# Optimization experiments

Hardware: AMD Instinct MI355X
Metric: run time of the kernel (lower is better)

Reference implementation:

```python
import jax, jax.numpy as jnp
import numpy as np

N = 100000
E = 1600000
IN_C, HID_C, OUT_C = 64, 128, 64


def sage_conv(x, edge_index, W_l, b_l, W_r):
    # PyG SAGEConv (mean aggr): out = lin_l(mean_{j in N(i)} x_j) + lin_r(x_i)
    src, dst = edge_index[0], edge_index[1]
    n = x.shape[0]
    msg = x[src]                                        # [E, C] gather
    agg = jax.ops.segment_sum(msg, dst, num_segments=n) # [N, C] scatter-add
    deg = jax.ops.segment_sum(jnp.ones((msg.shape[0],), x.dtype), dst, num_segments=n)
    agg = agg / jnp.maximum(deg, 1.0)[:, None]          # mean, deg-0 safe
    return agg @ W_l.T + b_l + x @ W_r.T


def setup_inputs() -> dict:
    key = jax.random.key(0)
    ks = jax.random.split(key, 8)
    x = jax.random.normal(ks[0], (N, IN_C), dtype=jnp.float32)
    edge_index = jax.random.randint(ks[1], (2, E), 0, N)
    s1 = 1.0 / np.sqrt(IN_C)
    s2 = 1.0 / np.sqrt(HID_C)
    W1_l = jax.random.uniform(ks[2], (HID_C, IN_C), jnp.float32, -s1, s1)
    W1_r = jax.random.uniform(ks[3], (HID_C, IN_C), jnp.float32, -s1, s1)
    b1 = jax.random.uniform(ks[4], (HID_C,), jnp.float32, -s1, s1)
    W2_l = jax.random.uniform(ks[5], (OUT_C, HID_C), jnp.float32, -s2, s2)
    W2_r = jax.random.uniform(ks[6], (OUT_C, HID_C), jnp.float32, -s2, s2)
    b2 = jax.random.uniform(ks[7], (OUT_C,), jnp.float32, -s2, s2)
    return {"x": x, "edge_index": edge_index, "W1_l": W1_l, "W1_r": W1_r,
            "b1": b1, "W2_l": W2_l, "W2_r": W2_r, "b2": b2}


def reference(x, edge_index, W1_l, W1_r, b1, W2_l, W2_r, b2):
    h = sage_conv(x, edge_index, W1_l, b1, W1_r)
    h = jax.nn.relu(h)
    h = sage_conv(h, edge_index, W2_l, b2, W2_r)
    return jax.nn.sigmoid(h)
```

## Files before the change

kernel.cpp:

```cpp
#include <hip/hip_runtime.h>
#include <math.h>

#define IN_C 64
#define HID_C 128
#define OUT_C 64
#define NBK 256
#define BD 64
#define GS 16

typedef __attribute__((ext_vector_type(8))) short bf16x8;
typedef __attribute__((ext_vector_type(4))) float f32x4;

__device__ __forceinline__ unsigned short f2bf(float f) {
  unsigned u = __float_as_uint(f);
  u = (u + 0x7FFFu + ((u >> 16) & 1u)) >> 16;
  return (unsigned short)u;
}
__device__ __forceinline__ float bf2f(unsigned v) {
  return __uint_as_float(v << 16);
}
__device__ __forceinline__ unsigned pack2(float a, float b) {
  return (unsigned)f2bf(a) | ((unsigned)f2bf(b) << 16);
}

__global__ __launch_bounds__(256) void k_xb(const int* __restrict__ dst,
                                            int* __restrict__ bh,
                                            const float4* __restrict__ x4,
                                            uint2* __restrict__ xh2,
                                            int E, int Mreal, int Mtot) {
  __shared__ int hh[NBK];
  int t = threadIdx.x;
  if (blockIdx.x < 1024) {
    hh[t] = 0;
    __syncthreads();
    for (int e = blockIdx.x * 256 + t; e < E; e += 1024 * 256)
      atomicAdd(&hh[dst[e] >> 9], 1);
    __syncthreads();
    if (hh[t]) atomicAdd(&bh[t * GS], hh[t]);
  } else {
    int b = blockIdx.x - 1024;
    for (int i = b * 256 + t; i < Mtot; i += 2048 * 256) {
      uint2 p = {0u, 0u};
      if (i < Mreal) {
        float4 v = x4[i];
        p.x = pack2(v.x, v.y);
        p.y = pack2(v.z, v.w);
      }
      xh2[i] = p;
    }
  }
}

__global__ __launch_bounds__(256) void k_bscan(const int* __restrict__ bh,
                                               int* __restrict__ bstart,
                                               int* __restrict__ rstart,
                                               int* __restrict__ gcur) {
  __shared__ int s1[NBK], s2[NBK];
  int t = threadIdx.x;
  int cnt = bh[t * GS];
  int region = 16 * min(cnt, (cnt >> 4) + 512);
  int creg = cnt + 4096;
  s1[t] = region; s2[t] = creg;
  __syncthreads();
  for (int off = 1; off < NBK; off <<= 1) {
    int a1 = (t >= off) ? s1[t - off] : 0;
    int a2 = (t >= off) ? s2[t - off] : 0;
    __syncthreads();
    s1[t] += a1; s2[t] += a2;
    __syncthreads();
  }
  int ex1 = s1[t] - region;
  int ex2 = s2[t] - creg;
  bstart[t] = ex1; gcur[t * GS] = ex1; rstart[t] = ex2;
}

__global__ __launch_bounds__(256) void k_msplit(const int* __restrict__ src,
                                                const int* __restrict__ dst,
                                                int* __restrict__ gcur,
                                                int* __restrict__ ebuf, int E) {
  __shared__ int bcnt[NBK], bhead[NBK];
  __shared__ int bins[BD][NBK];
  int t = threadIdx.x;
  bcnt[t] = 0; bhead[t] = 0;
  int per = (E + gridDim.x - 1) / gridDim.x;
  int e0 = blockIdx.x * per, e1 = min(E, e0 + per);
  int e = e0 + t;
  int pb[8], pv[8]; int pc = 0;
  __syncthreads();
  for (;;) {
    while (pc < 8 && e < e1) {
      int d = dst[e], s = src[e];
      pb[pc] = d >> 9; pv[pc] = (s << 9) | (d & 511);
      pc++; e += 256;
    }
    for (int q = pc - 1; q >= 0; --q) {
      int pos = atomicAdd(&bcnt[pb[q]], 1);
      if (pos < BD) {
        bins[(bhead[pb[q]] + pos) & (BD - 1)][pb[q]] = pv[q];
        pc--;
        if (q != pc) { pb[q] = pb[pc]; pv[q] = pv[pc]; }
      }
    }
    int pending = __syncthreads_count(pc > 0 || e < e1);
    int cntv = min(bcnt[t], BD);
    int head = bhead[t];
    while (cntv >= 16) {
      int base = atomicAdd(&gcur[t * GS], 16);
      int4 o[4];
#pragma unroll
      for (int k = 0; k < 16; ++k)
        ((int*)o)[k] = bins[(head + k) & (BD - 1)][t];
      int4* g = (int4*)(ebuf + base);
      g[0] = o[0]; g[1] = o[1]; g[2] = o[2]; g[3] = o[3];
      head = (head + 16) & (BD - 1);
      cntv -= 16;
    }
    bhead[t] = head;
    bcnt[t] = cntv;
    __syncthreads();
    if (!pending) break;
  }
  int cntv = bcnt[t];
  if (cntv > 0) {
    int head = bhead[t];
    int base = atomicAdd(&gcur[t * GS], 16);
#pragma unroll
    for (int k = 0; k < 16; ++k)
      ebuf[base + k] = (k < cntv) ? bins[(head + k) & (BD - 1)][t] : -1;
  }
}

__global__ __launch_bounds__(512) void k_localcsr(const int* __restrict__ ebuf,
                                                  const int* __restrict__ bstart,
                                                  const int* __restrict__ gcur,
                                                  const int* __restrict__ rstart,
                                                  int* __restrict__ csr,
                                                  int* __restrict__ row_start,
                                                  int* __restrict__ rend,
                                                  float* __restrict__ invd, int N) {
  __shared__ int lcnt[512], loff[512], lcur[512];
  int t = threadIdx.x, b = blockIdx.x;
  int start = bstart[b], endp = gcur[b * GS], rs = rstart[b];
  lcnt[t] = 0;
  __syncthreads();
  for (int i = start + t; i < endp; i += 512) {
    int pe = ebuf[i];
    if (pe != -1) atomicAdd(&lcnt[pe & 511], 1);
  }
  __syncthreads();
  int v = lcnt[t];
  int pvn = (v + 7) & ~7;
  loff[t] = pvn;
  __syncthreads();
  for (int off = 1; off < 512; off <<= 1) {
    int a = (t >= off) ? loff[t - off] : 0;
    __syncthreads();
    loff[t] += a;
    __syncthreads();
  }
  int ex = loff[t] - pvn;
  lcur[t] = ex;
  int node = (b << 9) + t;
  if (node < N) {
    row_start[node] = rs + ex;
    rend[node] = rs + ex + pvn;
    invd[node] = 1.0f / fmaxf((float)v, 1.0f);
  }
  __syncthreads();
  for (int i = start + t; i < endp; i += 512) {
    int pe = ebuf[i];
    if (pe != -1) {
      int pos = atomicAdd(&lcur[pe & 511], 1);
      csr[rs + pos] = pe >> 9;
    }
  }
  for (int k = ex + v; k < ex + pvn; ++k) csr[rs + k] = N;
}

__global__ __launch_bounds__(256) void k_gather1(const uint4* __restrict__ xh4,
                                                 const int* __restrict__ csr,
                                                 const int* __restrict__ row_start,
                                                 const int* __restrict__ rend,
                                                 const float* __restrict__ invd,
                                                 uint4* __restrict__ aggh4, int N) {
  int node = (blockIdx.x * 256 + threadIdx.x) >> 3;
  if (node >= N) return;
  int c = threadIdx.x & 7;
  int lb = threadIdx.x & 56;
  int j = row_start[node], end = rend[node];
  float a0 = 0, a1 = 0, a2 = 0, a3 = 0, a4 = 0, a5 = 0, a6 = 0, a7 = 0;
  for (; j < end; j += 8) {
    int sv = csr[j + c];
#pragma unroll
    for (int k = 0; k < 8; ++k) {
      int s = __shfl(sv, lb + k);
      uint4 v = xh4[s * 8 + c];
      a0 += bf2f(v.x & 0xffffu); a1 += bf2f(v.x >> 16);
      a2 += bf2f(v.y & 0xffffu); a3 += bf2f(v.y >> 16);
      a4 += bf2f(v.z & 0xffffu); a5 += bf2f(v.z >> 16);
      a6 += bf2f(v.w & 0xffffu); a7 += bf2f(v.w >> 16);
    }
  }
  float inv = invd[node];
  uint4 p;
  p.x = pack2(a0 * inv, a1 * inv);
  p.y = pack2(a2 * inv, a3 * inv);
  p.z = pack2(a4 * inv, a5 * inv);
  p.w = pack2(a6 * inv, a7 * inv);
  aggh4[node * 8 + c] = p;
}

__global__ __launch_bounds__(512, 4) void k_lin12(
    const uint4* __restrict__ aggh4, const uint4* __restrict__ xh4,
    const float* __restrict__ W1l, const float* __restrict__ W1r,
    const float* __restrict__ b1, const float* __restrict__ W2l,
    const float* __restrict__ W2r, const float* __restrict__ b2,
    unsigned short* __restrict__ zh, float* __restrict__ r, int N) {
  __shared__ __align__(16) char sA[128 * 256];
  __shared__ __align__(16) char sH[128 * 256];
  int t = threadIdx.x;
  if (blockIdx.x == 0 && t < 32) ((unsigned*)zh)[N * 32 + t] = 0;
  int w = t >> 6, lane = t & 63, qm = lane >> 4, ln = lane & 15;
  bf16x8 w1f[4], w2f[4];
  int o = w * 16 + ln;
#pragma unroll
  for (int kc = 0; kc < 4; ++kc) {
    int k0 = kc * 32 + qm * 8;
    bf16x8 v1, v2;
#pragma unroll
    for (int j = 0; j < 8; ++j) {
      int kk = k0 + j;
      float f1 = (kk < 64) ? W1l[o * 64 + kk] : W1r[o * 64 + (kk - 64)];
      float f2 = (o < 64) ? W2l[o * 128 + kk] : W2r[(o - 64) * 128 + kk];
      v1[j] = (short)f2bf(f1);
      v2[j] = (short)f2bf(f2);
    }
    w1f[kc] = v1; w2f[kc] = v2;
  }
  float4 b1v = *(const float4*)(b1 + w * 16 + qm * 4);
  int u = w * 16 + qm * 4;
  float4 b2v = {0.f, 0.f, 0.f, 0.f};
  if (u >= 64) b2v = *(const float4*)(b2 + (u - 64));

  int ntiles = (N + 127) >> 7;
  for (int tile = blockIdx.x; tile < ntiles; tile += gridDim.x) {
    int base = tile << 7;
#pragma unroll
    for (int rep = 0; rep < 4; ++rep) {
      int i = rep * 512 + t;
      int row = i >> 4, ch = i & 15;
      int node = base + row;
      uint4 v = {0u, 0u, 0u, 0u};
      if (node < N) v = (ch < 8) ? aggh4[node * 8 + ch] : xh4[node * 8 + (ch - 8)];
      *(uint4*)(sA + row * 256 + ((ch * 16) ^ ((row & 7) << 4))) = v;
    }
    __syncthreads();
#pragma unroll
    for (int g = 0; g < 8; ++g) {
      int row = g * 16 + ln;
      int rb = row * 256, sw = (row & 7) << 4;
      f32x4 acc = {0.f, 0.f, 0.f, 0.f};
#pragma unroll
      for (int kc = 0; kc < 4; ++kc) {
        bf16x8 af = *(const bf16x8*)(sA + rb + ((kc * 64 + qm * 16) ^ sw));
        acc = __builtin_amdgcn_mfma_f32_16x16x32_bf16(w1f[kc], af, acc, 0, 0, 0);
      }
      uint2 hp;
      hp.x = pack2(fmaxf(acc[0] + b1v.x, 0.f), fmaxf(acc[1] + b1v.y, 0.f));
      hp.y = pack2(fmaxf(acc[2] + b1v.z, 0.f), fmaxf(acc[3] + b1v.w, 0.f));
      *(uint2*)(sH + rb + ((w * 32 + qm * 8) ^ sw)) = hp;
    }
    __syncthreads();
#pragma unroll
    for (int g = 0; g < 8; ++g) {
      int row = g * 16 + ln;
      int rb = row * 256, sw = (row & 7) << 4;
      f32x4 acc = {0.f, 0.f, 0.f, 0.f};
#pragma unroll
      for (int kc = 0; kc < 4; ++kc) {
        bf16x8 hf = *(const bf16x8*)(sH + rb + ((kc * 64 + qm * 16) ^ sw));
        acc = __builtin_amdgcn_mfma_f32_16x16x32_bf16(w2f[kc], hf, acc, 0, 0, 0);
      }
      int node = base + row;
      if (node < N) {
        if (u < 64) {
          uint2 zv;
          zv.x = pack2(acc[0], acc[1]);
          zv.y = pack2(acc[2], acc[3]);
          *(uint2*)(zh + node * 64 + u) = zv;
        } else {
          float4 rv;
          rv.x = acc[0] + b2v.x; rv.y = acc[1] + b2v.y;
          rv.z = acc[2] + b2v.z; rv.w = acc[3] + b2v.w;
          *(float4*)(r + node * 64 + (u - 64)) = rv;
        }
      }
    }
    __syncthreads();
  }
}

__global__ __launch_bounds__(256) void k_gather2b(const uint4* __restrict__ zh4,
                                                  const float* __restrict__ r,
                                                  const int* __restrict__ csr,
                                                  const int* __restrict__ row_start,
                                                  const int* __restrict__ rend,
                                                  const float* __restrict__ invd,
                                                  float* __restrict__ out, int N) {
  int node = (blockIdx.x * 256 + threadIdx.x) >> 3;
  if (node >= N) return;
  int c = threadIdx.x & 7;
  int lb = threadIdx.x & 56;
  int j = row_start[node], end = rend[node];
  float a0 = 0, a1 = 0, a2 = 0, a3 = 0, a4 = 0, a5 = 0, a6 = 0, a7 = 0;
  for (; j < end; j += 8) {
    int sv = csr[j + c];
#pragma unroll
    for (int k = 0; k < 8; ++k) {
      int s = __shfl(sv, lb + k);
      uint4 v = zh4[s * 8 + c];
      a0 += bf2f(v.x & 0xffffu); a1 += bf2f(v.x >> 16);
      a2 += bf2f(v.y & 0xffffu); a3 += bf2f(v.y >> 16);
      a4 += bf2f(v.z & 0xffffu); a5 += bf2f(v.z >> 16);
      a6 += bf2f(v.w & 0xffffu); a7 += bf2f(v.w >> 16);
    }
  }
  float inv = invd[node];
  const float4* r4 = (const float4*)r;
  float4* o4 = (float4*)out;
  int bi = node * 16 + c * 2;
  float4 r0 = r4[bi], r1 = r4[bi + 1];
  float4 w0, w1;
  w0.x = 1.0f / (1.0f + __expf(-(a0 * inv + r0.x)));
  w0.y = 1.0f / (1.0f + __expf(-(a1 * inv + r0.y)));
  w0.z = 1.0f / (1.0f + __expf(-(a2 * inv + r0.z)));
  w0.w = 1.0f / (1.0f + __expf(-(a3 * inv + r0.w)));
  w1.x = 1.0f / (1.0f + __expf(-(a4 * inv + r1.x)));
  w1.y = 1.0f / (1.0f + __expf(-(a5 * inv + r1.y)));
  w1.z = 1.0f / (1.0f + __expf(-(a6 * inv + r1.z)));
  w1.w = 1.0f / (1.0f + __expf(-(a7 * inv + r1.w)));
  o4[bi] = w0;
  o4[bi + 1] = w1;
}

extern "C" void kernel_launch(void* const* d_in, const int* in_sizes, int n_in,
                              void* d_out, int out_size, void* d_ws, size_t ws_size,
                              hipStream_t stream) {
  const float* x   = (const float*)d_in[0];
  const int*   ei  = (const int*)d_in[1];
  const float* W1l = (const float*)d_in[2];
  const float* W1r = (const float*)d_in[3];
  const float* b1  = (const float*)d_in[4];
  const float* W2l = (const float*)d_in[5];
  const float* W2r = (const float*)d_in[6];
  const float* b2  = (const float*)d_in[7];
  float* out = (float*)d_out;

  int N = in_sizes[0] / IN_C;
  int E = in_sizes[1] / 2;
  const int* src = ei;
  const int* dst = ei + E;

  char* ws = (char*)d_ws;
  size_t off = 0;
  auto alignup = [](size_t v) { return (v + 511) & ~(size_t)511; };
  int* bh = (int*)(ws + off);         off = alignup(off + NBK * GS * 4);
  int* gcur = (int*)(ws + off);       off = alignup(off + NBK * GS * 4);
  int* bstart = (int*)(ws + off);     off = alignup(off + NBK * 4);
  int* rstart = (int*)(ws + off);     off = alignup(off + NBK * 4);
  int* csr = (int*)(ws + off);        off = alignup(off + ((size_t)E + NBK * 4096) * 4);
  int* row_start = (int*)(ws + off);  off = alignup(off + (size_t)N * 4);
  int* rend = (int*)(ws + off);       off = alignup(off + (size_t)N * 4);
  float* invd = (float*)(ws + off);   off = alignup(off + (size_t)N * 4);
  unsigned short* xh = (unsigned short*)(ws + off);   off = alignup(off + (size_t)(N + 1) * 64 * 2);
  unsigned short* aggh = (unsigned short*)(ws + off); off = alignup(off + (size_t)N * 64 * 2);
  unsigned short* zh = (unsigned short*)(ws + off);   off = alignup(off + (size_t)(N + 1) * 64 * 2);
  float* rbuf = (float*)(ws + off);   off = alignup(off + (size_t)N * 64 * 4);
  int* ebuf = (int*)aggh;

  hipMemsetAsync(bh, 0, NBK * GS * 4, stream);
  k_xb<<<3072, 256, 0, stream>>>(dst, bh, (const float4*)x, (uint2*)xh,
                                 E, N * 16, (N + 1) * 16);
  k_bscan<<<1, NBK, 0, stream>>>(bh, bstart, rstart, gcur);
  k_msplit<<<512, 256, 0, stream>>>(src, dst, gcur, ebuf, E);
  k_localcsr<<<NBK, 512, 0, stream>>>(ebuf, bstart, gcur, rstart, csr,
                                      row_start, rend, invd, N);

  k_gather1<<<(N + 31) / 32, 256, 0, stream>>>((const uint4*)xh, csr, row_start,
                                               rend, invd, (uint4*)aggh, N);
  k_lin12<<<512, 512, 0, stream>>>((const uint4*)aggh, (const uint4*)xh,
                                   W1l, W1r, b1, W2l, W2r, b2, zh, rbuf, N);
  k_gather2b<<<(N + 31) / 32, 256, 0, stream>>>((const uint4*)zh, rbuf, csr,
                                                row_start, rend, invd, out, N);
}
```

Baseline: 277.1 us.

## Precompute bf16 weights and load MFMA operands directly from global in lin12

Weight conversion to bf16 moves into extra blocks of the first preprocessing kernel, so each lin12 block loads ready-made bf16 fragments instead of converting fp32 weights itself. lin12 now runs one 128-row tile per block, with no grid-stride loop. It reads its A fragments straight from global memory into registers, skipping the swizzled LDS staging buffer, and only stages the hidden layer in a padded LDS array. Nontemporal loads and stores are added for the aggregated features, the r buffer and the output. The changes trade LDS traffic and barriers for uncoalesced-ish direct global fragment loads, and the last tile reads rows past N without a bounds check.

Measured after the change: 274.1 us. No clear change (-1.1%).

```diff
diff --git a/kernel.cpp b/kernel.cpp
--- a/kernel.cpp
+++ b/kernel.cpp
@@ -10,6 +10,7 @@
 
 typedef __attribute__((ext_vector_type(8))) short bf16x8;
 typedef __attribute__((ext_vector_type(4))) float f32x4;
+typedef __attribute__((ext_vector_type(4))) unsigned u32x4;
 
 __device__ __forceinline__ unsigned short f2bf(float f) {
   unsigned u = __float_as_uint(f);
@@ -27,6 +28,12 @@
                                             int* __restrict__ bh,
                                             const float4* __restrict__ x4,
                                             uint2* __restrict__ xh2,
+                                            const float* __restrict__ W1l,
+                                            const float* __restrict__ W1r,
+                                            const float* __restrict__ W2l,
+                                            const float* __restrict__ W2r,
+                                            unsigned short* __restrict__ w1h,
+                                            unsigned short* __restrict__ w2h,
                                             int E, int Mreal, int Mtot) {
   __shared__ int hh[NBK];
   int t = threadIdx.x;
@@ -37,7 +44,7 @@
       atomicAdd(&hh[dst[e] >> 9], 1);
     __syncthreads();
     if (hh[t]) atomicAdd(&bh[t * GS], hh[t]);
-  } else {
+  } else if (blockIdx.x < 3072) {
     int b = blockIdx.x - 1024;
     for (int i = b * 256 + t; i < Mtot; i += 2048 * 256) {
       uint2 p = {0u, 0u};
@@ -47,6 +54,13 @@
         p.y = pack2(v.z, v.w);
       }
       xh2[i] = p;
+    }
+  } else {
+    int idx = (blockIdx.x - 3072) * 256 + t;
+    for (int i = idx; i < 128 * 128; i += 32 * 256) {
+      int o = i >> 7, k = i & 127;
+      w1h[i] = f2bf((k < 64) ? W1l[o * 64 + k] : W1r[o * 64 + (k - 64)]);
+      w2h[i] = f2bf((o < 64) ? W2l[o * 128 + k] : W2r[(o - 64) * 128 + k]);
     }
   }
 }
@@ -182,7 +196,7 @@
                                                  const int* __restrict__ row_start,
                                                  const int* __restrict__ rend,
                                                  const float* __restrict__ invd,
-                                                 uint4* __restrict__ aggh4, int N) {
+                                                 unsigned* __restrict__ aggh_u, int N) {
   int node = (blockIdx.x * 256 + threadIdx.x) >> 3;
   if (node >= N) return;
   int c = threadIdx.x & 7;
@@ -202,101 +216,81 @@
     }
   }
   float inv = invd[node];
-  uint4 p;
+  u32x4 p;
   p.x = pack2(a0 * inv, a1 * inv);
   p.y = pack2(a2 * inv, a3 * inv);
   p.z = pack2(a4 * inv, a5 * inv);
   p.w = pack2(a6 * inv, a7 * inv);
-  aggh4[node * 8 + c] = p;
+  __builtin_nontemporal_store(p, (u32x4*)(aggh_u + (size_t)node * 32 + c * 4));
 }
 
 __global__ __launch_bounds__(512, 4) void k_lin12(
     const uint4* __restrict__ aggh4, const uint4* __restrict__ xh4,
-    const float* __restrict__ W1l, const float* __restrict__ W1r,
-    const float* __restrict__ b1, const float* __restrict__ W2l,
-    const float* __restrict__ W2r, const float* __restrict__ b2,
+    const unsigned short* __restrict__ w1h, const unsigned short* __restrict__ w2h,
+    const float* __restrict__ b1, const float* __restrict__ b2,
     unsigned short* __restrict__ zh, float* __restrict__ r, int N) {
-  __shared__ __align__(16) char sA[128 * 256];
-  __shared__ __align__(16) char sH[128 * 256];
+  __shared__ __align__(16) unsigned short sH[128 * 136];
   int t = threadIdx.x;
   if (blockIdx.x == 0 && t < 32) ((unsigned*)zh)[N * 32 + t] = 0;
   int w = t >> 6, lane = t & 63, qm = lane >> 4, ln = lane & 15;
+  int o = w * 16 + ln;
   bf16x8 w1f[4], w2f[4];
-  int o = w * 16 + ln;
 #pragma unroll
   for (int kc = 0; kc < 4; ++kc) {
-    int k0 = kc * 32 + qm * 8;
-    bf16x8 v1, v2;
-#pragma unroll
-    for (int j = 0; j < 8; ++j) {
-      int kk = k0 + j;
-      float f1 = (kk < 64) ? W1l[o * 64 + kk] : W1r[o * 64 + (kk - 64)];
-      float f2 = (o < 64) ? W2l[o * 128 + kk] : W2r[(o - 64) * 128 + kk];
-      v1[j] = (short)f2bf(f1);
-      v2[j] = (short)f2bf(f2);
-    }
-    w1f[kc] = v1; w2f[kc] = v2;
+    w1f[kc] = *(const bf16x8*)(w1h + o * 128 + kc * 32 + qm * 8);
+    w2f[kc] = *(const bf16x8*)(w2h + o * 128 + kc * 32 + qm * 8);
   }
   float4 b1v = *(const float4*)(b1 + w * 16 + qm * 4);
   int u = w * 16 + qm * 4;
   float4 b2v = {0.f, 0.f, 0.f, 0.f};
   if (u >= 64) b2v = *(const float4*)(b2 + (u - 64));
 
-  int ntiles = (N + 127) >> 7;
-  for (int tile = blockIdx.x; tile < ntiles; tile += gridDim.x) {
-    int base = tile << 7;
-#pragma unroll
-    for (int rep = 0; rep < 4; ++rep) {
-      int i = rep * 512 + t;
-      int row = i >> 4, ch = i & 15;
-      int node = base + row;
-      uint4 v = {0u, 0u, 0u, 0u};
-      if (node < N) v = (ch < 8) ? aggh4[node * 8 + ch] : xh4[node * 8 + (ch - 8)];
-      *(uint4*)(sA + row * 256 + ((ch * 16) ^ ((row & 7) << 4))) = v;
-    }
-    __syncthreads();
-#pragma unroll
-    for (int g = 0; g < 8; ++g) {
-      int row = g * 16 + ln;
-      int rb = row * 256, sw = (row & 7) << 4;
-      f32x4 acc = {0.f, 0.f, 0.f, 0.f};
-#pragma unroll
-      for (int kc = 0; kc < 4; ++kc) {
-        bf16x8 af = *(const bf16x8*)(sA + rb + ((kc * 64 + qm * 16) ^ sw));
-        acc = __builtin_amdgcn_mfma_f32_16x16x32_bf16(w1f[kc], af, acc, 0, 0, 0);
+  int base = (int)blockIdx.x << 7;
+#pragma unroll 2
+  for (int g = 0; g < 8; ++g) {
+    int node = base + g * 16 + ln;
+    bf16x8 af[4];
+#pragma unroll
+    for (int kc = 0; kc < 4; ++kc) {
+      int ch = kc * 4 + qm;
+      af[kc] = (ch < 8) ? *(const bf16x8*)&aggh4[node * 8 + ch]
+                        : *(const bf16x8*)&xh4[node * 8 + (ch - 8)];
+    }
+    f32x4 acc = {0.f, 0.f, 0.f, 0.f};
+#pragma unroll
+    for (int kc = 0; kc < 4; ++kc)
+      acc = __builtin_amdgcn_mfma_f32_16x16x32_bf16(w1f[kc], af[kc], acc, 0, 0, 0);
+    uint2 hp;
+    hp.x = pack2(fmaxf(acc[0] + b1v.x, 0.f), fmaxf(acc[1] + b1v.y, 0.f));
+    hp.y = pack2(fmaxf(acc[2] + b1v.z, 0.f), fmaxf(acc[3] + b1v.w, 0.f));
+    *(uint2*)(sH + (g * 16 + ln) * 136 + w * 16 + qm * 4) = hp;
+  }
+  __syncthreads();
+#pragma unroll 2
+  for (int g = 0; g < 8; ++g) {
+    int row = g * 16 + ln;
+    bf16x8 hf[4];
+#pragma unroll
+    for (int kc = 0; kc < 4; ++kc)
+      hf[kc] = *(const bf16x8*)(sH + row * 136 + kc * 32 + qm * 8);
+    f32x4 acc = {0.f, 0.f, 0.f, 0.f};
+#pragma unroll
+    for (int kc = 0; kc < 4; ++kc)
+      acc = __builtin_amdgcn_mfma_f32_16x16x32_bf16(w2f[kc], hf[kc], acc, 0, 0, 0);
+    int node = base + row;
+    if (node < N) {
+      if (u < 64) {
+        uint2 zv;
+        zv.x = pack2(acc[0], acc[1]);
+        zv.y = pack2(acc[2], acc[3]);
+        *(uint2*)(zh + node * 64 + u) = zv;
+      } else {
+        f32x4 rv;
+        rv.x = acc[0] + b2v.x; rv.y = acc[1] + b2v.y;
+        rv.z = acc[2] + b2v.z; rv.w = acc[3] + b2v.w;
+        __builtin_nontemporal_store(rv, (f32x4*)(r + node * 64 + (u - 64)));
       }
-      uint2 hp;
-      hp.x = pack2(fmaxf(acc[0] + b1v.x, 0.f), fmaxf(acc[1] + b1v.y, 0.f));
-      hp.y = pack2(fmaxf(acc[2] + b1v.z, 0.f), fmaxf(acc[3] + b1v.w, 0.f));
-      *(uint2*)(sH + rb + ((w * 32 + qm * 8) ^ sw)) = hp;
-    }
-    __syncthreads();
-#pragma unroll
-    for (int g = 0; g < 8; ++g) {
-      int row = g * 16 + ln;
-      int rb = row * 256, sw = (row & 7) << 4;
-      f32x4 acc = {0.f, 0.f, 0.f, 0.f};
-#pragma unroll
-      for (int kc = 0; kc < 4; ++kc) {
-        bf16x8 hf = *(const bf16x8*)(sH + rb + ((kc * 64 + qm * 16) ^ sw));
-        acc = __builtin_amdgcn_mfma_f32_16x16x32_bf16(w2f[kc], hf, acc, 0, 0, 0);
-      }
-      int node = base + row;
-      if (node < N) {
-        if (u < 64) {
-          uint2 zv;
-          zv.x = pack2(acc[0], acc[1]);
-          zv.y = pack2(acc[2], acc[3]);
-          *(uint2*)(zh + node * 64 + u) = zv;
-        } else {
-          float4 rv;
-          rv.x = acc[0] + b2v.x; rv.y = acc[1] + b2v.y;
-          rv.z = acc[2] + b2v.z; rv.w = acc[3] + b2v.w;
-          *(float4*)(r + node * 64 + (u - 64)) = rv;
-        }
-      }
-    }
-    __syncthreads();
+    }
   }
 }
 
@@ -326,11 +320,12 @@
     }
   }
   float inv = invd[node];
-  const float4* r4 = (const float4*)r;
-  float4* o4 = (float4*)out;
+  const f32x4* r4 = (const f32x4*)r;
+  f32x4* o4 = (f32x4*)out;
   int bi = node * 16 + c * 2;
-  float4 r0 = r4[bi], r1 = r4[bi + 1];
-  float4 w0, w1;
+  f32x4 r0 = __builtin_nontemporal_load(&r4[bi]);
+  f32x4 r1 = __builtin_nontemporal_load(&r4[bi + 1]);
+  f32x4 w0, w1;
   w0.x = 1.0f / (1.0f + __expf(-(a0 * inv + r0.x)));
   w0.y = 1.0f / (1.0f + __expf(-(a1 * inv + r0.y)));
   w0.z = 1.0f / (1.0f + __expf(-(a2 * inv + r0.z)));
@@ -339,8 +334,8 @@
   w1.y = 1.0f / (1.0f + __expf(-(a5 * inv + r1.y)));
   w1.z = 1.0f / (1.0f + __expf(-(a6 * inv + r1.z)));
   w1.w = 1.0f / (1.0f + __expf(-(a7 * inv + r1.w)));
-  o4[bi] = w0;
-  o4[bi + 1] = w1;
+  __builtin_nontemporal_store(w0, &o4[bi]);
+  __builtin_nontemporal_store(w1, &o4[bi + 1]);
 }
 
 extern "C" void kernel_launch(void* const* d_in, const int* in_sizes, int n_in,
@@ -372,6 +367,8 @@
   int* row_start = (int*)(ws + off);  off = alignup(off + (size_t)N * 4);
   int* rend = (int*)(ws + off);       off = alignup(off + (size_t)N * 4);
   float* invd = (float*)(ws + off);   off = alignup(off + (size_t)N * 4);
+  unsigned short* w1h = (unsigned short*)(ws + off);  off = alignup(off + 128 * 128 * 2);
+  unsigned short* w2h = (unsigned short*)(ws + off);  off = alignup(off + 128 * 128 * 2);
   unsigned short* xh = (unsigned short*)(ws + off);   off = alignup(off + (size_t)(N + 1) * 64 * 2);
   unsigned short* aggh = (unsigned short*)(ws + off); off = alignup(off + (size_t)N * 64 * 2);
   unsigned short* zh = (unsigned short*)(ws + off);   off = alignup(off + (size_t)(N + 1) * 64 * 2);
@@ -379,7 +376,8 @@
   int* ebuf = (int*)aggh;
 
   hipMemsetAsync(bh, 0, NBK * GS * 4, stream);
-  k_xb<<<3072, 256, 0, stream>>>(dst, bh, (const float4*)x, (uint2*)xh,
+  k_xb<<<3104, 256, 0, stream>>>(dst, bh, (const float4*)x, (uint2*)xh,
+                                 W1l, W1r, W2l, W2r, w1h, w2h,
                                  E, N * 16, (N + 1) * 16);
   k_bscan<<<1, NBK, 0, stream>>>(bh, bstart, rstart, gcur);
   k_msplit<<<512, 256, 0, stream>>>(src, dst, gcur, ebuf, E);
@@ -387,9 +385,9 @@
                                       row_start, rend, invd, N);
 
   k_gather1<<<(N + 31) / 32, 256, 0, stream>>>((const uint4*)xh, csr, row_start,
-                                               rend, invd, (uint4*)aggh, N);
-  k_lin12<<<512, 512, 0, stream>>>((const uint4*)aggh, (const uint4*)xh,
-                                   W1l, W1r, b1, W2l, W2r, b2, zh, rbuf, N);
+                                               rend, invd, (unsigned*)aggh, N);
+  k_lin12<<<(N + 127) / 128, 512, 0, stream>>>((const uint4*)aggh, (const uint4*)xh,
+                                               w1h, w2h, b1, b2, zh, rbuf, N);
   k_gather2b<<<(N + 31) / 32, 256, 0, stream>>>((const uint4*)zh, rbuf, csr,
                                                 row_start, rend, invd, out, N);
 }
```
